# Kernel tuning notes

Measured on AMD Instinct MI355X. Metric: run time of the kernel, lower is better.

Reference implementation:

```python
import jax, jax.numpy as jnp
import numpy as np
from jax import lax

B, T, D = 2, 2048, 2048
H, DK, DV = 16, 128, 128
K = 4  # conv kernel size
KEY_DIM = H * DK      # 2048
VAL_DIM = H * DV      # 2048
CONV_DIM = 2 * KEY_DIM + VAL_DIM  # 6144
EPS = 1e-6


def setup_inputs() -> dict:
    key = jax.random.key(0)
    ks = jax.random.split(key, 10)
    s = lambda fan: 1.0 / np.sqrt(fan)
    return {
        "hidden_states": jax.random.normal(ks[0], (B, T, D), jnp.float32),
        "W_qkv": jax.random.normal(ks[1], (D, CONV_DIM), jnp.float32) * s(D),
        "conv_w": jax.random.normal(ks[2], (CONV_DIM, 1, K), jnp.float32) * s(K),
        "W_z": jax.random.normal(ks[3], (D, VAL_DIM), jnp.float32) * s(D),
        "W_b": jax.random.normal(ks[4], (D, H), jnp.float32) * s(D),
        "W_a": jax.random.normal(ks[5], (D, H), jnp.float32) * s(D),
        "dt_bias": jnp.ones((H,), jnp.float32),
        "A_log": jnp.log(jax.random.uniform(ks[6], (H,), jnp.float32, 1e-3, 16.0)),
        "norm_weight": jnp.ones((DV,), jnp.float32),
        "W_out": jax.random.normal(ks[7], (VAL_DIM, D), jnp.float32) * s(VAL_DIM),
    }


def _l2norm(x):
    return x * lax.rsqrt(jnp.sum(x * x, axis=-1, keepdims=True) + 1e-6)


def _gated_delta_rule(q, k, v, g, beta):
    """q,k: [B,T,H,DK]; v: [B,T,H,DV]; g,beta: [B,T,H]. Returns o: [B,T,H,DV]."""
    # time-major for scan
    qT, kT, vT = (jnp.moveaxis(x, 1, 0) for x in (q, k, v))  # [T,B,H,d]
    gT = jnp.moveaxis(g, 1, 0)      # [T,B,H]
    bT = jnp.moveaxis(beta, 1, 0)   # [T,B,H]

    def step(S, inp):
        q_t, k_t, v_t, g_t, b_t = inp
        S = S * jnp.exp(g_t)[..., None, None]                      # decay [B,H,DK,DV]
        kv_mem = jnp.einsum("bhk,bhkv->bhv", k_t, S)               # S^T k
        delta = (v_t - kv_mem) * b_t[..., None]                     # beta-scaled error
        S = S + jnp.einsum("bhk,bhv->bhkv", k_t, delta)
        o_t = jnp.einsum("bhk,bhkv->bhv", q_t, S)
        return S, o_t

    S0 = jnp.zeros((q.shape[0], H, DK, DV), q.dtype)
    _, oT = lax.scan(step, S0, (qT, kT, vT, gT, bT))
    return jnp.moveaxis(oT, 0, 1)  # [B,T,H,DV]


def reference(hidden_states, W_qkv, conv_w, W_z, W_b, W_a, dt_bias, A_log,
              norm_weight, W_out):
    Bs, Ts, _ = hidden_states.shape

    # qkv projection + depthwise causal conv1d + silu
    mixed = hidden_states @ W_qkv                      # [B,T,CONV_DIM]
    xc = jnp.moveaxis(mixed, 1, 2)                     # [B,C,T]
    xc = lax.conv_general_dilated(xc, conv_w, (1,), [(K - 1, 0)],
                                  feature_group_count=CONV_DIM)
    mixed = jax.nn.silu(jnp.moveaxis(xc, 1, 2))        # [B,T,C]

    q, k, v = jnp.split(mixed, [KEY_DIM, 2 * KEY_DIM], axis=-1)
    q = _l2norm(q.reshape(Bs, Ts, H, DK)) * (DK ** -0.5)
    k = _l2norm(k.reshape(Bs, Ts, H, DK))
    v = v.reshape(Bs, Ts, H, DV)

    beta = jax.nn.sigmoid(hidden_states @ W_b)                     # [B,T,H]
    g = -jnp.exp(A_log) * jax.nn.softplus(hidden_states @ W_a + dt_bias)

    o = _gated_delta_rule(q, k, v, g, beta)            # [B,T,H,DV]

    # gated RMSNorm (Mamba2-style: gate first, then normalize)
    z = (hidden_states @ W_z).reshape(Bs, Ts, H, DV)
    o = o * jax.nn.silu(z)
    var = jnp.mean(o * o, axis=-1, keepdims=True)
    o = o * lax.rsqrt(var + EPS) * norm_weight

    return o.reshape(Bs, Ts, VAL_DIM) @ W_out          # [B,T,D]
```

## Files before the change

### kernel.cpp

```cpp
#include <hip/hip_runtime.h>

#define B_ 2
#define T_ 2048
#define D_ 2048
#define H_ 16
#define CONV_DIM_ 6144
#define NC_ 32
#define CK_ 64

typedef __bf16 bf16;
typedef bf16 bf16x8 __attribute__((ext_vector_type(8)));
typedef bf16 bf16x4 __attribute__((ext_vector_type(4)));
typedef float floatx4 __attribute__((ext_vector_type(4)));

__device__ __forceinline__ void async_copy16(bf16* lds, const bf16* g) {
    auto* g1 = (const __attribute__((address_space(1))) unsigned int*)g;
    auto* l3 = (__attribute__((address_space(3))) unsigned int*)lds;
    __builtin_amdgcn_global_load_lds(g1, l3, 16, 0, 0);
}

__global__ void cvt_bf16_kernel(const float* __restrict__ in, bf16* __restrict__ out, int n4) {
    int i = blockIdx.x * 256 + threadIdx.x;
    if (i < n4) {
        float4 v = ((const float4*)in)[i];
        bf16x4 o = { (bf16)v.x, (bf16)v.y, (bf16)v.z, (bf16)v.w };
        *(bf16x4*)(out + 4 * (size_t)i) = o;
    }
}

__global__ void transpose_kernel(const float* __restrict__ in, bf16* __restrict__ out, int R, int Cn) {
    __shared__ float tile[32][33];
    const int c0 = blockIdx.x << 5, r0 = blockIdx.y << 5;
    const int tx = threadIdx.x & 31, ty = threadIdx.x >> 5;
#pragma unroll
    for (int i = 0; i < 4; ++i) {
        int r = ty + (i << 3);
        tile[r][tx] = in[(size_t)(r0 + r) * Cn + c0 + tx];
    }
    __syncthreads();
#pragma unroll
    for (int i = 0; i < 4; ++i) {
        int cc = ty + (i << 3);
        out[(size_t)(c0 + cc) * R + r0 + tx] = (bf16)tile[tx][cc];
    }
}

__global__ void wba_cvt_kernel(const float* __restrict__ Wb, const float* __restrict__ Wa,
                               bf16* __restrict__ Wba) {
    int idx = blockIdx.x * 256 + threadIdx.x;
    int d = idx >> 4, h = idx & 15;
    Wba[(size_t)h * 2048 + d]        = (bf16)Wb[idx];
    Wba[(size_t)(h + 16) * 2048 + d] = (bf16)Wa[idx];
}

template <typename OutT>
__global__ __launch_bounds__(256) void gemm_kernel(
    const bf16* __restrict__ A, const bf16* __restrict__ Bt, OutT* __restrict__ C,
    int M, int N, int K) {
    __shared__ bf16 As[128 * 64];
    __shared__ bf16 Bs[128 * 64];
    const int tid = threadIdx.x;
    const int m0 = blockIdx.y << 7;
    const int n0 = blockIdx.x << 7;
    const int wave = tid >> 6, lane = tid & 63;
    const int wm = (wave >> 1) << 6, wn = (wave & 1) << 6;
    const int lrow = lane & 15, quad = lane >> 4;
    const int rl = lane >> 3;
    const int c8s = (lane & 7) ^ (rl & 7);

    floatx4 acc[4][4];
#pragma unroll
    for (int mt = 0; mt < 4; ++mt)
#pragma unroll
        for (int nt = 0; nt < 4; ++nt)
            acc[mt][nt] = floatx4{0.f, 0.f, 0.f, 0.f};

    for (int k0 = 0; k0 < K; k0 += 64) {
        __syncthreads();
#pragma unroll
        for (int i = 0; i < 4; ++i) {
            const int slot = wave * 4 + i;
            const int r = slot * 8 + rl;
            async_copy16(&As[slot * 512], A + (size_t)(m0 + r) * K + k0 + c8s * 8);
            async_copy16(&Bs[slot * 512], Bt + (size_t)(n0 + r) * K + k0 + c8s * 8);
        }
        __syncthreads();
#pragma unroll
        for (int kk = 0; kk < 64; kk += 32) {
            const int sw = (((kk >> 3) + quad) ^ (lrow & 7)) << 3;
            bf16x8 af[4], bfr[4];
#pragma unroll
            for (int mt = 0; mt < 4; ++mt) {
                af[mt]  = *(const bf16x8*)(&As[((wm + (mt << 4) + lrow) << 6) + sw]);
                bfr[mt] = *(const bf16x8*)(&Bs[((wn + (mt << 4) + lrow) << 6) + sw]);
            }
#pragma unroll
            for (int mt = 0; mt < 4; ++mt)
#pragma unroll
                for (int nt = 0; nt < 4; ++nt)
                    acc[mt][nt] = __builtin_amdgcn_mfma_f32_16x16x32_bf16(af[mt], bfr[nt], acc[mt][nt], 0, 0, 0);
        }
    }
#pragma unroll
    for (int mt = 0; mt < 4; ++mt)
#pragma unroll
        for (int nt = 0; nt < 4; ++nt) {
            const int col = n0 + wn + (nt << 4) + lrow;
            const int rowb = m0 + wm + (mt << 4) + (quad << 2);
#pragma unroll
            for (int i2 = 0; i2 < 4; ++i2)
                C[(size_t)(rowb + i2) * N + col] = (OutT)acc[mt][nt][i2];
        }
}

__global__ __launch_bounds__(512, 2) void gemm256_kernel(
    const bf16* __restrict__ A, const bf16* __restrict__ Bt,
    bf16* __restrict__ C0, bf16* __restrict__ C1,
    int M, int Ncat, int K, int split, int ld0, int ld1) {
    __shared__ bf16 As[4][256 * 32];
    __shared__ bf16 Bs[4][256 * 32];
    const int tid = threadIdx.x;
    const int wave = tid >> 6, lane = tid & 63;
    const int quad = lane >> 4, lrow = lane & 15;
    const int wm = (wave >> 2) << 7;
    const int wn = (wave & 3) << 6;
    const int m0 = blockIdx.y << 8, n0 = blockIdx.x << 8;

    const bf16* gA[2];
    const bf16* gB[2];
#pragma unroll
    for (int i = 0; i < 2; ++i) {
        const int q = wave * 2 + i;
        const int u = (lane & 7) ^ (lane >> 3);
        const int row = (q * 8 + (lane >> 3)) * 2 + (u >> 2);
        const int col = (u & 3) * 8;
        gA[i] = A  + (size_t)(m0 + row) * K + col;
        gB[i] = Bt + (size_t)(n0 + row) * K + col;
    }

    auto loff = [](int row, int qd) -> int {
        return ((row >> 1) << 6) + (((((row & 1) << 2) | qd) ^ ((row >> 1) & 7)) << 3);
    };

    floatx4 acc[8][4];
#pragma unroll
    for (int mt = 0; mt < 8; ++mt)
#pragma unroll
        for (int nt = 0; nt < 4; ++nt)
            acc[mt][nt] = floatx4{0.f, 0.f, 0.f, 0.f};

    const int KT = K >> 5;

#pragma unroll
    for (int t = 0; t < 3; ++t) {
        async_copy16(&As[t][(wave * 2 + 0) * 512], gA[0] + t * 32);
        async_copy16(&As[t][(wave * 2 + 1) * 512], gA[1] + t * 32);
        async_copy16(&Bs[t][(wave * 2 + 0) * 512], gB[0] + t * 32);
        async_copy16(&Bs[t][(wave * 2 + 1) * 512], gB[1] + t * 32);
    }
    asm volatile("s_waitcnt vmcnt(8)" ::: "memory");
    __builtin_amdgcn_s_barrier();

    for (int t = 0; t < KT; ++t) {
        const int b = t & 3;
        const bf16* as = &As[b][0];
        const bf16* bs = &Bs[b][0];
        bf16x8 bfr[4], af[4];
#pragma unroll
        for (int nt = 0; nt < 4; ++nt)
            bfr[nt] = *(const bf16x8*)(bs + loff(wn + nt * 16 + lrow, quad));
#pragma unroll
        for (int mt = 0; mt < 4; ++mt)
            af[mt] = *(const bf16x8*)(as + loff(wm + mt * 16 + lrow, quad));
        if (t + 2 < KT)       asm volatile("s_waitcnt vmcnt(4)" ::: "memory");
        else if (t + 2 == KT) asm volatile("s_waitcnt vmcnt(0)" ::: "memory");
        if (t + 3 < KT) {
            const int bn = (t + 3) & 3;
            async_copy16(&As[bn][(wave * 2 + 0) * 512], gA[0] + (t + 3) * 32);
            async_copy16(&As[bn][(wave * 2 + 1) * 512], gA[1] + (t + 3) * 32);
        }
        __builtin_amdgcn_s_barrier();
        asm volatile("s_waitcnt lgkmcnt(0)" ::: "memory");
        __builtin_amdgcn_sched_barrier(0);
        __builtin_amdgcn_s_setprio(1);
#pragma unroll
        for (int mt = 0; mt < 4; ++mt)
#pragma unroll
            for (int nt = 0; nt < 4; ++nt)
                acc[mt][nt] = __builtin_amdgcn_mfma_f32_16x16x32_bf16(
                    af[mt], bfr[nt], acc[mt][nt], 0, 0, 0);
        __builtin_amdgcn_s_setprio(0);
        __builtin_amdgcn_sched_barrier(0);
        __builtin_amdgcn_s_barrier();
#pragma unroll
        for (int mt = 0; mt < 4; ++mt)
            af[mt] = *(const bf16x8*)(as + loff(wm + 64 + mt * 16 + lrow, quad));
        if (t + 3 < KT) {
            const int bn = (t + 3) & 3;
            async_copy16(&Bs[bn][(wave * 2 + 0) * 512], gB[0] + (t + 3) * 32);
            async_copy16(&Bs[bn][(wave * 2 + 1) * 512], gB[1] + (t + 3) * 32);
        }
        __builtin_amdgcn_s_barrier();
        asm volatile("s_waitcnt lgkmcnt(0)" ::: "memory");
        __builtin_amdgcn_sched_barrier(0);
        __builtin_amdgcn_s_setprio(1);
#pragma unroll
        for (int mt = 0; mt < 4; ++mt)
#pragma unroll
            for (int nt = 0; nt < 4; ++nt)
                acc[4 + mt][nt] = __builtin_amdgcn_mfma_f32_16x16x32_bf16(
                    af[mt], bfr[nt], acc[4 + mt][nt], 0, 0, 0);
        __builtin_amdgcn_s_setprio(0);
        __builtin_amdgcn_sched_barrier(0);
        __builtin_amdgcn_s_barrier();
    }

    const bool second = (n0 >= split);
    bf16* Cp = second ? C1 : C0;
    const int ldc = second ? ld1 : ld0;
    const int nc0 = second ? n0 - split : n0;
#pragma unroll
    for (int mt = 0; mt < 8; ++mt)
#pragma unroll
        for (int nt = 0; nt < 4; ++nt) {
            const int col = nc0 + wn + nt * 16 + lrow;
            const int rowb = m0 + wm + mt * 16 + (quad << 2);
#pragma unroll
            for (int i2 = 0; i2 < 4; ++i2)
                Cp[(size_t)(rowb + i2) * ldc + col] = (bf16)acc[mt][nt][i2];
        }
}

__global__ void conv_silu_kernel(const bf16* __restrict__ mixed, const float* __restrict__ cw,
                                 bf16* __restrict__ qb, bf16* __restrict__ kb, bf16* __restrict__ vb) {
    const int s = blockIdx.x;
    const int bt = blockIdx.y;
    const int t = bt & (T_ - 1);
    const int b = bt >> 11;
    const int c = (s << 7) + threadIdx.x;
    const size_t base = (size_t)bt * CONV_DIM_ + c;
    const float w0 = cw[c * 4], w1 = cw[c * 4 + 1], w2 = cw[c * 4 + 2], w3 = cw[c * 4 + 3];
    float acc = (float)mixed[base] * w3;
    if (t >= 1) acc += (float)mixed[base - CONV_DIM_] * w2;
    if (t >= 2) acc += (float)mixed[base - 2 * CONV_DIM_] * w1;
    if (t >= 3) acc += (float)mixed[base - 3 * CONV_DIM_] * w0;
    const float val = acc / (1.f + __expf(-acc));

    __shared__ float red[2];
    if (s < 32) {
        float ss = val * val;
#pragma unroll
        for (int o = 1; o < 64; o <<= 1) ss += __shfl_xor(ss, o);
        if ((threadIdx.x & 63) == 0) red[threadIdx.x >> 6] = ss;
        __syncthreads();
        const float scale = rsqrtf(red[0] + red[1] + 1e-6f);
        const int h = s & 15;
        const size_t oidx = (((size_t)(b * H_ + h)) * T_ + t) * 128 + threadIdx.x;
        if (s < 16) qb[oidx] = (bf16)(val * scale * 0.08838834764831845f);
        else        kb[oidx] = (bf16)(val * scale);
    } else {
        const int h = s - 32;
        const size_t oidx = (((size_t)(b * H_ + h)) * T_ + t) * 128 + threadIdx.x;
        vb[oidx] = (bf16)val;
    }
}

__global__ __launch_bounds__(256) void gbeta_mfma_kernel(
    const bf16* __restrict__ Xb, const bf16* __restrict__ Wba,
    const float* __restrict__ dtb, const float* __restrict__ Alog,
    float* __restrict__ gbuf, float* __restrict__ bbuf) {
    const int tid = threadIdx.x, wave = tid >> 6, lane = tid & 63;
    const int ln = lane & 15, qd = lane >> 4;
    const int m0 = blockIdx.x * 64 + wave * 16;
    floatx4 acc0 = {0.f, 0.f, 0.f, 0.f}, acc1 = {0.f, 0.f, 0.f, 0.f};
    const bf16* arow = Xb + (size_t)(m0 + ln) * 2048 + qd * 8;
    const bf16* b0 = Wba + (size_t)ln * 2048 + qd * 8;
    const bf16* b1 = Wba + (size_t)(16 + ln) * 2048 + qd * 8;
    for (int k = 0; k < 2048; k += 32) {
        bf16x8 af  = *(const bf16x8*)(arow + k);
        bf16x8 bf0 = *(const bf16x8*)(b0 + k);
        bf16x8 bf1 = *(const bf16x8*)(b1 + k);
        acc0 = __builtin_amdgcn_mfma_f32_16x16x32_bf16(af, bf0, acc0, 0, 0, 0);
        acc1 = __builtin_amdgcn_mfma_f32_16x16x32_bf16(af, bf1, acc1, 0, 0, 0);
    }
    const float dtbv = dtb[ln], al = __expf(Alog[ln]);
#pragma unroll
    for (int ii = 0; ii < 4; ++ii) {
        const int row = m0 + qd * 4 + ii;
        const int t = row & (T_ - 1), b = row >> 11;
        const size_t o = ((size_t)(b * H_ + ln)) * T_ + t;
        bbuf[o] = 1.f / (1.f + __expf(-acc0[ii]));
        const float xx = acc1[ii] + dtbv;
        const float sp = (xx > 15.f) ? xx : log1pf(__expf(xx));
        gbuf[o] = -al * sp;
    }
}

__global__ __launch_bounds__(256) void qkkt_kernel(const bf16* __restrict__ qb, const bf16* __restrict__ kb,
                                                   float* __restrict__ Araw, float* __restrict__ Mraw) {
    const int u = blockIdx.x;
    const int bh = u >> 5, nc = u & 31;
    const int t0 = nc * CK_;
    const int tid = threadIdx.x, wave = tid >> 6, lane = tid & 63;
    const int qd = lane >> 4, ln = lane & 15;
    __shared__ bf16 Kc[64 * 136], Qc[64 * 136];
    const size_t kbase = ((size_t)bh * T_ + t0) * 128;
#pragma unroll
    for (int it = 0; it < 4; ++it) {
        int idx = it * 256 + tid;
        int row = idx >> 4, c8 = idx & 15;
        *(uint4*)(&Kc[row * 136 + c8 * 8]) = *(const uint4*)(kb + kbase + row * 128 + c8 * 8);
        *(uint4*)(&Qc[row * 136 + c8 * 8]) = *(const uint4*)(qb + kbase + row * 128 + c8 * 8);
    }
    __syncthreads();
#pragma unroll
    for (int nt = 0; nt < 4; ++nt) {
        floatx4 accA = {0.f, 0.f, 0.f, 0.f}, accM = {0.f, 0.f, 0.f, 0.f};
#pragma unroll
        for (int kk = 0; kk < 4; ++kk) {
            bf16x8 bfr = *(const bf16x8*)(&Kc[(nt * 16 + ln) * 136 + kk * 32 + qd * 8]);
            bf16x8 afK = *(const bf16x8*)(&Kc[(wave * 16 + ln) * 136 + kk * 32 + qd * 8]);
            bf16x8 afQ = *(const bf16x8*)(&Qc[(wave * 16 + ln) * 136 + kk * 32 + qd * 8]);
            accA = __builtin_amdgcn_mfma_f32_16x16x32_bf16(afK, bfr, accA, 0, 0, 0);
            accM = __builtin_amdgcn_mfma_f32_16x16x32_bf16(afQ, bfr, accM, 0, 0, 0);
        }
#pragma unroll
        for (int ii = 0; ii < 4; ++ii) {
            int i = wave * 16 + qd * 4 + ii, j = nt * 16 + ln;
            Araw[(size_t)u * 4096 + i * 64 + j] = accA[ii];
            Mraw[(size_t)u * 4096 + i * 64 + j] = accM[ii];
        }
    }
}

__global__ __launch_bounds__(64) void prep_kernel(
    const float* __restrict__ gbuf, const float* __restrict__ bbuf,
    const float* __restrict__ Araw, const float* __restrict__ Mraw,
    float* __restrict__ lamg, float* __restrict__ ratiog,
    bf16* __restrict__ Tg, bf16* __restrict__ Mg) {
    const int u = blockIdx.x, bh = u >> 5, nc = u & 31, t0 = nc * CK_;
    const int lane = threadIdx.x;
    __shared__ float L[64 * 65];
    __shared__ float cv[64], bv[64];
    float g = gbuf[(size_t)bh * T_ + t0 + lane];
    float beta = bbuf[(size_t)bh * T_ + t0 + lane];
    float c = g;
#pragma unroll
    for (int off = 1; off < 64; off <<= 1) {
        float tval = __shfl_up(c, off);
        if (lane >= off) c += tval;
    }
    float c63 = __shfl(c, 63);
    lamg[(size_t)u * 64 + lane] = __expf(c);
    ratiog[(size_t)u * 64 + lane] = __expf(c63 - c);
    cv[lane] = c; bv[lane] = beta;
    __syncthreads();
    for (int i = 0; i < 64; ++i) {
        float a = Araw[(size_t)u * 4096 + i * 64 + lane];
        L[i * 65 + lane] = (lane < i) ? bv[i] * __expf(cv[i] - c) * a : 0.f;
    }
    __syncthreads();
    float t[64];
#pragma unroll
    for (int i = 0; i < 64; ++i) t[i] = (i == lane) ? 1.f : 0.f;
#pragma unroll
    for (int j = 0; j < 63; ++j) {
#pragma unroll
        for (int i = j + 1; i < 64; ++i)
            t[i] -= L[i * 65 + j] * t[j];
    }
#pragma unroll
    for (int i = 0; i < 64; ++i)
        Tg[(size_t)u * 4096 + i * 64 + lane] = (bf16)t[i];
    for (int i = 0; i < 64; ++i) {
        float m = Mraw[(size_t)u * 4096 + i * 64 + lane];
        float mij = (lane <= i) ? __expf(cv[i] - c) * m : 0.f;
        Mg[(size_t)u * 4096 + i * 64 + lane] = (bf16)mij;
    }
}

struct Pref {
    uint4 t2[2], m2[2];
    bf16x8 kf[4], qf[4];
    bf16x8 ktf[2][2];
    float rrv[4], vv[4], lam[4], bet[4], lamlast;
};

__device__ __forceinline__ void load_pref(
    Pref& p, int u, int t0, size_t kbase, int tid, int wave, int ln, int qd,
    int bh, int vbase,
    const bf16* __restrict__ qb, const bf16* __restrict__ kb, const bf16* __restrict__ vb,
    const bf16* __restrict__ Tg, const bf16* __restrict__ Mg,
    const float* __restrict__ lamg, const float* __restrict__ ratiog,
    const float* __restrict__ bbuf) {
#pragma unroll
    for (int it = 0; it < 2; ++it) {
        int idx = it * 256 + tid;
        int row = idx >> 3, c8 = idx & 7;
        p.t2[it] = *(const uint4*)(Tg + (size_t)u * 4096 + row * 64 + c8 * 8);
        p.m2[it] = *(const uint4*)(Mg + (size_t)u * 4096 + row * 64 + c8 * 8);
    }
    const size_t rowoff = kbase + (size_t)(wave * 16 + ln) * 128;
#pragma unroll
    for (int kk = 0; kk < 4; ++kk) {
        p.kf[kk] = *(const bf16x8*)(kb + rowoff + kk * 32 + qd * 8);
        p.qf[kk] = *(const bf16x8*)(qb + rowoff + kk * 32 + qd * 8);
    }
#pragma unroll
    for (int mt = 0; mt < 2; ++mt) {
        const int kd = (wave * 2 + mt) * 16 + ln;
#pragma unroll
        for (int kk2 = 0; kk2 < 2; ++kk2) {
            const int ib = kk2 * 32 + qd * 8;
#pragma unroll
            for (int j = 0; j < 8; ++j)
                p.ktf[mt][kk2][j] = kb[kbase + (size_t)(ib + j) * 128 + kd];
        }
    }
    const int i0 = wave * 16 + qd * 4;
#pragma unroll
    for (int ii = 0; ii < 4; ++ii) {
        p.vv[ii]  = (float)vb[kbase + (size_t)(i0 + ii) * 128 + vbase + ln];
        p.lam[ii] = lamg[(size_t)u * 64 + i0 + ii];
        p.bet[ii] = bbuf[(size_t)bh * T_ + t0 + i0 + ii];
        p.rrv[ii] = ratiog[(size_t)u * 64 + i0 + ii];
    }
    p.lamlast = lamg[(size_t)u * 64 + 63];
}

__global__ __launch_bounds__(256) void seq_kernel(
    const bf16* __restrict__ qb, const bf16* __restrict__ kb, const bf16* __restrict__ vb,
    const bf16* __restrict__ Tg, const bf16* __restrict__ Mg,
    const float* __restrict__ lamg, const float* __restrict__ ratiog,
    const float* __restrict__ bbuf, float* __restrict__ ob) {
    const int bh = blockIdx.x & 31;
    const int vs = blockIdx.x >> 5;
    const int vbase = vs * 16;
    const int tid = threadIdx.x;
    const int wave = tid >> 6, lane = tid & 63;
    const int qd = lane >> 4, ln = lane & 15;

    __shared__ bf16 Tt[64 * 72], Mm[64 * 72];
    __shared__ bf16 bT[16 * 72], Dt[16 * 72], Dtr[16 * 72];
    __shared__ bf16 Sbf[16 * 136];
    __shared__ float Sf[16 * 132];

    for (int idx = tid; idx < 16 * 132; idx += 256) Sf[idx] = 0.f;
    for (int idx = tid; idx < 16 * 136; idx += 256) Sbf[idx] = (bf16)0.f;

    Pref cur, nxt;
    load_pref(cur, bh * NC_, 0, (size_t)bh * T_ * 128, tid, wave, ln, qd, bh, vbase,
              qb, kb, vb, Tg, Mg, lamg, ratiog, bbuf);
    __syncthreads();

    for (int nc = 0; nc < NC_; ++nc) {
        const int t0 = nc * CK_;
        const size_t kbase = ((size_t)bh * T_ + t0) * 128;

#pragma unroll
        for (int it = 0; it < 2; ++it) {
            int idx = it * 256 + tid;
            int row = idx >> 3, c8 = idx & 7;
            *(uint4*)(&Tt[row * 72 + c8 * 8]) = cur.t2[it];
            *(uint4*)(&Mm[row * 72 + c8 * 8]) = cur.m2[it];
        }

        {
            const int ncn = (nc + 1 < NC_) ? nc + 1 : nc;
            load_pref(nxt, bh * NC_ + ncn, ncn * CK_, ((size_t)bh * T_ + (size_t)ncn * CK_) * 128,
                      tid, wave, ln, qd, bh, vbase, qb, kb, vb, Tg, Mg, lamg, ratiog, bbuf);
        }

        floatx4 ks = {0.f, 0.f, 0.f, 0.f};
#pragma unroll
        for (int kk = 0; kk < 4; ++kk) {
            bf16x8 bf = *(const bf16x8*)(&Sbf[ln * 136 + kk * 32 + qd * 8]);
            ks = __builtin_amdgcn_mfma_f32_16x16x32_bf16(cur.kf[kk], bf, ks, 0, 0, 0);
        }
        {
            const int i0 = wave * 16 + qd * 4;
            bf16x4 bw;
#pragma unroll
            for (int ii = 0; ii < 4; ++ii)
                bw[ii] = (bf16)(cur.bet[ii] * (cur.vv[ii] - cur.lam[ii] * ks[ii]));
            *(bf16x4*)(&bT[ln * 72 + i0]) = bw;
        }
        __syncthreads();

        {
            floatx4 acc = {0.f, 0.f, 0.f, 0.f};
#pragma unroll
            for (int kk = 0; kk < 2; ++kk) {
                bf16x8 af = *(const bf16x8*)(&Tt[(wave * 16 + ln) * 72 + kk * 32 + qd * 8]);
                bf16x8 bf = *(const bf16x8*)(&bT[ln * 72 + kk * 32 + qd * 8]);
                acc = __builtin_amdgcn_mfma_f32_16x16x32_bf16(af, bf, acc, 0, 0, 0);
            }
            const int i0 = wave * 16 + qd * 4;
            bf16x4 dw = { (bf16)acc[0], (bf16)acc[1], (bf16)acc[2], (bf16)acc[3] };
            *(bf16x4*)(&Dt[ln * 72 + i0]) = dw;
            bf16x4 dwr = { (bf16)(acc[0] * cur.rrv[0]), (bf16)(acc[1] * cur.rrv[1]),
                           (bf16)(acc[2] * cur.rrv[2]), (bf16)(acc[3] * cur.rrv[3]) };
            *(bf16x4*)(&Dtr[ln * 72 + i0]) = dwr;
        }
        __syncthreads();

        {
            floatx4 acc = {0.f, 0.f, 0.f, 0.f};
#pragma unroll
            for (int kk = 0; kk < 4; ++kk) {
                bf16x8 bf = *(const bf16x8*)(&Sbf[ln * 136 + kk * 32 + qd * 8]);
                acc = __builtin_amdgcn_mfma_f32_16x16x32_bf16(cur.qf[kk], bf, acc, 0, 0, 0);
            }
            floatx4 o;
#pragma unroll
            for (int ii = 0; ii < 4; ++ii) o[ii] = acc[ii] * cur.lam[ii];
#pragma unroll
            for (int kk = 0; kk < 2; ++kk) {
                bf16x8 af = *(const bf16x8*)(&Mm[(wave * 16 + ln) * 72 + kk * 32 + qd * 8]);
                bf16x8 bf = *(const bf16x8*)(&Dt[ln * 72 + kk * 32 + qd * 8]);
                o = __builtin_amdgcn_mfma_f32_16x16x32_bf16(af, bf, o, 0, 0, 0);
            }
            const int i0 = wave * 16 + qd * 4;
#pragma unroll
            for (int ii = 0; ii < 4; ++ii)
                ob[kbase + (size_t)(i0 + ii) * 128 + vbase + ln] = o[ii];
        }
#pragma unroll
        for (int mt = 0; mt < 2; ++mt) {
            const int kt = wave * 2 + mt;
            floatx4 acc = {0.f, 0.f, 0.f, 0.f};
#pragma unroll
            for (int kk = 0; kk < 2; ++kk) {
                bf16x8 bf = *(const bf16x8*)(&Dtr[ln * 72 + kk * 32 + qd * 8]);
                acc = __builtin_amdgcn_mfma_f32_16x16x32_bf16(cur.ktf[mt][kk], bf, acc, 0, 0, 0);
            }
            const int k0 = kt * 16 + qd * 4;
            floatx4 sold = *(floatx4*)(&Sf[ln * 132 + k0]);
#pragma unroll
            for (int ii = 0; ii < 4; ++ii) sold[ii] = sold[ii] * cur.lamlast + acc[ii];
            *(floatx4*)(&Sf[ln * 132 + k0]) = sold;
        }
        __syncthreads();
        {
            const int vloc = tid >> 4, k0 = (tid & 15) * 8;
            floatx4 s0 = *(floatx4*)(&Sf[vloc * 132 + k0]);
            floatx4 s1 = *(floatx4*)(&Sf[vloc * 132 + k0 + 4]);
            bf16x8 sb = { (bf16)s0[0], (bf16)s0[1], (bf16)s0[2], (bf16)s0[3],
                          (bf16)s1[0], (bf16)s1[1], (bf16)s1[2], (bf16)s1[3] };
            *(bf16x8*)(&Sbf[vloc * 136 + k0]) = sb;
        }
        __syncthreads();
        cur = nxt;
    }
}

__global__ void gated_norm_kernel(const float* __restrict__ ob, const bf16* __restrict__ z,
                                  const float* __restrict__ nw, bf16* __restrict__ onorm) {
    const int idx = blockIdx.x;
    const int h = idx & (H_ - 1);
    const int bt = idx >> 4;
    const int t = bt & (T_ - 1);
    const int b = bt >> 11;
    const int tid = threadIdx.x;
    const size_t obase = (((size_t)(b * H_ + h)) * T_ + t) * 128;
    const size_t zbase = (size_t)bt * 2048 + (h << 7);
    float o1 = ob[obase + tid], o2 = ob[obase + tid + 64];
    const float z1 = (float)z[zbase + tid], z2 = (float)z[zbase + tid + 64];
    o1 *= z1 / (1.f + __expf(-z1));
    o2 *= z2 / (1.f + __expf(-z2));
    float ss = o1 * o1 + o2 * o2;
#pragma unroll
    for (int o = 1; o < 64; o <<= 1) ss += __shfl_xor(ss, o);
    const float scale = rsqrtf(ss * (1.f / 128.f) + 1e-6f);
    onorm[zbase + tid]      = (bf16)(o1 * scale * nw[tid]);
    onorm[zbase + tid + 64] = (bf16)(o2 * scale * nw[tid + 64]);
}

extern "C" void kernel_launch(void* const* d_in, const int* in_sizes, int n_in,
                              void* d_out, int out_size, void* d_ws, size_t ws_size,
                              hipStream_t stream) {
    const float* X    = (const float*)d_in[0];
    const float* Wqkv = (const float*)d_in[1];
    const float* cw   = (const float*)d_in[2];
    const float* Wz   = (const float*)d_in[3];
    const float* Wb   = (const float*)d_in[4];
    const float* Wa   = (const float*)d_in[5];
    const float* dtb  = (const float*)d_in[6];
    const float* Alog = (const float*)d_in[7];
    const float* nw   = (const float*)d_in[8];
    const float* Wout = (const float*)d_in[9];
    float* out = (float*)d_out;

    char* ws = (char*)d_ws;
    size_t off = 0;
    auto alloc = [&](size_t bytes) -> char* {
        char* p = ws + off;
        off += (bytes + 255) & ~(size_t)255;
        return p;
    };
    bf16*  Xb      = (bf16*)alloc((size_t)B_ * T_ * D_ * 2);
    char*  wcat_p  = alloc((size_t)8192 * 2048 * 2);
    bf16*  Wcat    = (bf16*)wcat_p;
    bf16*  Woutt   = (bf16*)alloc((size_t)D_ * D_ * 2);
    bf16*  Wba     = (bf16*)alloc((size_t)32 * 2048 * 2);
    char*  mixed_p = alloc((size_t)B_ * T_ * CONV_DIM_ * 2);
    bf16*  mixedb  = (bf16*)mixed_p;
    bf16*  zb      = (bf16*)alloc((size_t)B_ * T_ * D_ * 2);
    bf16*  kbuf    = (bf16*)alloc((size_t)B_ * T_ * D_ * 2);
    bf16*  vbuf    = (bf16*)alloc((size_t)B_ * T_ * D_ * 2);
    float* gbuf    = (float*)alloc((size_t)B_ * T_ * H_ * 4);
    float* bbuf    = (float*)alloc((size_t)B_ * T_ * H_ * 4);
    float* Mraw    = (float*)alloc((size_t)1024 * 4096 * 4);
    bf16*  Tg      = (bf16*)alloc((size_t)1024 * 4096 * 2);
    bf16*  Mg      = (bf16*)alloc((size_t)1024 * 4096 * 2);
    float* lamg    = (float*)alloc((size_t)1024 * 64 * 4);
    float* ratiog  = (float*)alloc((size_t)1024 * 64 * 4);
    bf16*  qbuf    = (bf16*)wcat_p;
    float* obuf    = (float*)mixed_p;
    float* Araw    = (float*)(mixed_p + (size_t)B_ * T_ * D_ * 4);
    bf16*  onorm   = (bf16*)Xb;

    cvt_bf16_kernel<<<dim3((B_ * T_ * D_ / 4 + 255) / 256), dim3(256), 0, stream>>>(X, Xb, B_ * T_ * D_ / 4);
    transpose_kernel<<<dim3(CONV_DIM_ / 32, D_ / 32), dim3(256), 0, stream>>>(Wqkv, Wcat, D_, CONV_DIM_);
    transpose_kernel<<<dim3(D_ / 32, D_ / 32), dim3(256), 0, stream>>>(Wz, Wcat + (size_t)CONV_DIM_ * D_, D_, D_);
    transpose_kernel<<<dim3(D_ / 32, D_ / 32), dim3(256), 0, stream>>>(Wout, Woutt, D_, D_);
    wba_cvt_kernel<<<dim3(128), dim3(256), 0, stream>>>(Wb, Wa, Wba);

    gemm256_kernel<<<dim3(8192 / 256, B_ * T_ / 256), dim3(512), 0, stream>>>(
        Xb, Wcat, mixedb, zb, B_ * T_, 8192, D_, CONV_DIM_, CONV_DIM_, D_);

    gbeta_mfma_kernel<<<dim3(64), dim3(256), 0, stream>>>(Xb, Wba, dtb, Alog, gbuf, bbuf);
    conv_silu_kernel<<<dim3(CONV_DIM_ / 128, B_ * T_), dim3(128), 0, stream>>>(mixedb, cw, qbuf, kbuf, vbuf);

    qkkt_kernel<<<dim3(1024), dim3(256), 0, stream>>>(qbuf, kbuf, Araw, Mraw);
    prep_kernel<<<dim3(1024), dim3(64), 0, stream>>>(gbuf, bbuf, Araw, Mraw, lamg, ratiog, Tg, Mg);
    seq_kernel<<<dim3(256), dim3(256), 0, stream>>>(qbuf, kbuf, vbuf, Tg, Mg, lamg, ratiog, bbuf, obuf);

    gated_norm_kernel<<<dim3(B_ * T_ * H_), dim3(64), 0, stream>>>(obuf, zb, nw, onorm);

    gemm_kernel<float><<<dim3(D_ / 128, B_ * T_ / 128), dim3(256), 0, stream>>>(
        onorm, Woutt, out, B_ * T_, D_, D_);
}
```

Baseline: 643.1 us.

## Remap GEMM blocks per XCD, vectorize conv-silu, ping-pong seq prefetch buffers

Several unrelated changes land together. The 256-tile GEMM remaps block IDs so the blocks placed on each XCD share B-column tiles, which should improve L2 reuse. The conv+silu kernel now has each thread handle 8 channels with 16-byte loads and stores, and does the L2-norm reduction through 16-lane shuffles with no shared memory. The seq kernel unrolls its chunk loop by two and alternates between two prefetch structs, avoiding the struct copy, and it moves the strided kT gather to the end of the prefetch. The trade-offs are higher register pressure in seq_kernel and a block remap that hard-codes the current grid shape.

```diff
diff --git a/kernel.cpp b/kernel.cpp
--- a/kernel.cpp
+++ b/kernel.cpp
@@ -124,7 +124,11 @@
     const int quad = lane >> 4, lrow = lane & 15;
     const int wm = (wave >> 2) << 7;
     const int wn = (wave & 3) << 6;
-    const int m0 = blockIdx.y << 8, n0 = blockIdx.x << 8;
+    const int orig = blockIdx.y * gridDim.x + blockIdx.x;
+    const int xcd = orig & 7, pos = orig >> 3;
+    const int nblk = (xcd << 2) | (pos >> 4);
+    const int mblk = pos & 15;
+    const int m0 = mblk << 8, n0 = nblk << 8;
 
     const bf16* gA[2];
     const bf16* gB[2];
@@ -231,37 +235,57 @@
         }
 }
 
-__global__ void conv_silu_kernel(const bf16* __restrict__ mixed, const float* __restrict__ cw,
-                                 bf16* __restrict__ qb, bf16* __restrict__ kb, bf16* __restrict__ vb) {
-    const int s = blockIdx.x;
+__global__ __launch_bounds__(256) void conv_silu_kernel(
+    const bf16* __restrict__ mixed, const float* __restrict__ cw,
+    bf16* __restrict__ qb, bf16* __restrict__ kb, bf16* __restrict__ vb) {
     const int bt = blockIdx.y;
     const int t = bt & (T_ - 1);
     const int b = bt >> 11;
-    const int c = (s << 7) + threadIdx.x;
-    const size_t base = (size_t)bt * CONV_DIM_ + c;
-    const float w0 = cw[c * 4], w1 = cw[c * 4 + 1], w2 = cw[c * 4 + 2], w3 = cw[c * 4 + 3];
-    float acc = (float)mixed[base] * w3;
-    if (t >= 1) acc += (float)mixed[base - CONV_DIM_] * w2;
-    if (t >= 2) acc += (float)mixed[base - 2 * CONV_DIM_] * w1;
-    if (t >= 3) acc += (float)mixed[base - 3 * CONV_DIM_] * w0;
-    const float val = acc / (1.f + __expf(-acc));
-
-    __shared__ float red[2];
-    if (s < 32) {
-        float ss = val * val;
-#pragma unroll
-        for (int o = 1; o < 64; o <<= 1) ss += __shfl_xor(ss, o);
-        if ((threadIdx.x & 63) == 0) red[threadIdx.x >> 6] = ss;
-        __syncthreads();
-        const float scale = rsqrtf(red[0] + red[1] + 1e-6f);
-        const int h = s & 15;
-        const size_t oidx = (((size_t)(b * H_ + h)) * T_ + t) * 128 + threadIdx.x;
-        if (s < 16) qb[oidx] = (bf16)(val * scale * 0.08838834764831845f);
-        else        kb[oidx] = (bf16)(val * scale);
+    const int c0 = blockIdx.x * 2048 + threadIdx.x * 8;
+    const size_t base = (size_t)bt * CONV_DIM_ + c0;
+
+    bf16x8 zz;
+#pragma unroll
+    for (int j = 0; j < 8; ++j) zz[j] = (bf16)0.f;
+    const bf16x8 r3 = *(const bf16x8*)(mixed + base);
+    const bf16x8 r2 = (t >= 1) ? *(const bf16x8*)(mixed + base - CONV_DIM_) : zz;
+    const bf16x8 r1 = (t >= 2) ? *(const bf16x8*)(mixed + base - 2 * CONV_DIM_) : zz;
+    const bf16x8 r0 = (t >= 3) ? *(const bf16x8*)(mixed + base - 3 * CONV_DIM_) : zz;
+
+    const float4* cw4 = (const float4*)cw;
+    float vals[8];
+    float ss = 0.f;
+#pragma unroll
+    for (int j = 0; j < 8; ++j) {
+        const float4 w = cw4[c0 + j];
+        float acc = (float)r3[j] * w.w + (float)r2[j] * w.z +
+                    (float)r1[j] * w.y + (float)r0[j] * w.x;
+        const float sv = acc / (1.f + __expf(-acc));
+        vals[j] = sv;
+        ss += sv * sv;
+    }
+
+    if (c0 < 4096) {
+#pragma unroll
+        for (int o = 1; o < 16; o <<= 1) ss += __shfl_xor(ss, o);
+        const float scale = rsqrtf(ss + 1e-6f);
+        const bool isq = c0 < 2048;
+        const float mul = isq ? scale * 0.08838834764831845f : scale;
+        const int h = (c0 >> 7) & 15;
+        const int d0 = c0 & 127;
+        const size_t oidx = (((size_t)(b * H_ + h)) * T_ + t) * 128 + d0;
+        bf16x8 o8;
+#pragma unroll
+        for (int j = 0; j < 8; ++j) o8[j] = (bf16)(vals[j] * mul);
+        *(bf16x8*)((isq ? qb : kb) + oidx) = o8;
     } else {
-        const int h = s - 32;
-        const size_t oidx = (((size_t)(b * H_ + h)) * T_ + t) * 128 + threadIdx.x;
-        vb[oidx] = (bf16)val;
+        const int h = (c0 >> 7) & 15;
+        const int d0 = c0 & 127;
+        const size_t oidx = (((size_t)(b * H_ + h)) * T_ + t) * 128 + d0;
+        bf16x8 o8;
+#pragma unroll
+        for (int j = 0; j < 8; ++j) o8[j] = (bf16)vals[j];
+        *(bf16x8*)(vb + oidx) = o8;
     }
 }
 
@@ -406,17 +430,6 @@
         p.kf[kk] = *(const bf16x8*)(kb + rowoff + kk * 32 + qd * 8);
         p.qf[kk] = *(const bf16x8*)(qb + rowoff + kk * 32 + qd * 8);
     }
-#pragma unroll
-    for (int mt = 0; mt < 2; ++mt) {
-        const int kd = (wave * 2 + mt) * 16 + ln;
-#pragma unroll
-        for (int kk2 = 0; kk2 < 2; ++kk2) {
-            const int ib = kk2 * 32 + qd * 8;
-#pragma unroll
-            for (int j = 0; j < 8; ++j)
-                p.ktf[mt][kk2][j] = kb[kbase + (size_t)(ib + j) * 128 + kd];
-        }
-    }
     const int i0 = wave * 16 + qd * 4;
 #pragma unroll
     for (int ii = 0; ii < 4; ++ii) {
@@ -426,6 +439,17 @@
         p.rrv[ii] = ratiog[(size_t)u * 64 + i0 + ii];
     }
     p.lamlast = lamg[(size_t)u * 64 + 63];
+#pragma unroll
+    for (int mt = 0; mt < 2; ++mt) {
+        const int kd = (wave * 2 + mt) * 16 + ln;
+#pragma unroll
+        for (int kk2 = 0; kk2 < 2; ++kk2) {
+            const int ib = kk2 * 32 + qd * 8;
+#pragma unroll
+            for (int j = 0; j < 8; ++j)
+                p.ktf[mt][kk2][j] = kb[kbase + (size_t)(ib + j) * 128 + kd];
+        }
+    }
 }
 
 __global__ __launch_bounds__(256) void seq_kernel(
@@ -448,12 +472,7 @@
     for (int idx = tid; idx < 16 * 132; idx += 256) Sf[idx] = 0.f;
     for (int idx = tid; idx < 16 * 136; idx += 256) Sbf[idx] = (bf16)0.f;
 
-    Pref cur, nxt;
-    load_pref(cur, bh * NC_, 0, (size_t)bh * T_ * 128, tid, wave, ln, qd, bh, vbase,
-              qb, kb, vb, Tg, Mg, lamg, ratiog, bbuf);
-    __syncthreads();
-
-    for (int nc = 0; nc < NC_; ++nc) {
+    auto chunk_body = [&](Pref& cur, Pref& nxt, int nc) {
         const int t0 = nc * CK_;
         const size_t kbase = ((size_t)bh * T_ + t0) * 128;
 
@@ -550,7 +569,17 @@
             *(bf16x8*)(&Sbf[vloc * 136 + k0]) = sb;
         }
         __syncthreads();
-        cur = nxt;
+    };
+
+    Pref pA, pB;
+    load_pref(pA, bh * NC_, 0, (size_t)bh * T_ * 128, tid, wave, ln, qd, bh, vbase,
+              qb, kb, vb, Tg, Mg, lamg, ratiog, bbuf);
+    __syncthreads();
+
+#pragma unroll 1
+    for (int nc2 = 0; nc2 < NC_; nc2 += 2) {
+        chunk_body(pA, pB, nc2);
+        chunk_body(pB, pA, nc2 + 1);
     }
 }
 
@@ -630,7 +659,7 @@
         Xb, Wcat, mixedb, zb, B_ * T_, 8192, D_, CONV_DIM_, CONV_DIM_, D_);
 
     gbeta_mfma_kernel<<<dim3(64), dim3(256), 0, stream>>>(Xb, Wba, dtb, Alog, gbuf, bbuf);
-    conv_silu_kernel<<<dim3(CONV_DIM_ / 128, B_ * T_), dim3(128), 0, stream>>>(mixedb, cw, qbuf, kbuf, vbuf);
+    conv_silu_kernel<<<dim3(CONV_DIM_ / 2048, B_ * T_), dim3(256), 0, stream>>>(mixedb, cw, qbuf, kbuf, vbuf);
 
     qkkt_kernel<<<dim3(1024), dim3(256), 0, stream>>>(qbuf, kbuf, Araw, Mraw);
     prep_kernel<<<dim3(1024), dim3(64), 0, stream>>>(gbuf, bbuf, Araw, Mraw, lamg, ratiog, Tg, Mg);
```

Result: faster. 608.0 us (-5.5%).
